# Kernel optimization log

Hardware: AMD Instinct MI355X
Metric: run time of the kernel (lower is better)

Reference implementation:

```python
import jax, jax.numpy as jnp
import numpy as np

N_IN = 100000   # active voxels at coarse level
N_OUT = 400000  # active voxels at fine level
K = 8           # 2x2x2 kernel offsets of the inverse conv
P = 100000      # rulebook pairs per kernel offset
C_IN, C_OUT, C_SKIP = 128, 64, 64
EPS = 1e-5


def setup_inputs() -> dict:
    key = jax.random.key(0)
    k1, k2, k3, k4, k5, k6 = jax.random.split(key, 6)
    x_feats = jax.random.normal(k1, (N_IN, C_IN), jnp.float32)
    skip_feats = jax.random.normal(k2, (N_OUT, C_SKIP), jnp.float32)
    W_deconv = jax.random.normal(k3, (K, C_IN, C_OUT), jnp.float32) * (1.0 / np.sqrt(C_IN * K))
    gamma = jnp.ones((C_OUT,), jnp.float32)
    beta = jnp.zeros((C_OUT,), jnp.float32)
    W_fuse = jax.random.normal(k4, (C_OUT + C_SKIP, C_OUT), jnp.float32) * (1.0 / np.sqrt(C_OUT + C_SKIP))
    in_idx = jax.random.randint(k5, (K, P), 0, N_IN, jnp.int32)
    out_idx = jax.random.randint(k6, (K, P), 0, N_OUT, jnp.int32)
    return {"x_feats": x_feats, "skip_feats": skip_feats, "W_deconv": W_deconv,
            "gamma": gamma, "beta": beta, "W_fuse": W_fuse,
            "in_idx": in_idx, "out_idx": out_idx}


def reference(x_feats, skip_feats, W_deconv, gamma, beta, W_fuse, in_idx, out_idx):
    # --- SparseInverseConv3d: gather-GEMM-scatter over the rulebook ---
    gathered = x_feats[in_idx]                                  # [K,P,C_IN]
    contrib = jnp.einsum('kpi,kio->kpo', gathered, W_deconv)    # [K,P,C_OUT]
    y = jnp.zeros((N_OUT, C_OUT), x_feats.dtype)
    y = y.at[out_idx.reshape(-1)].add(contrib.reshape(-1, C_OUT))
    # --- BatchNorm1d (batch stats, biased var) + ReLU on voxel features ---
    mean = jnp.mean(y, axis=0)
    var = jnp.mean((y - mean) ** 2, axis=0)
    y = (y - mean) * jax.lax.rsqrt(var + EPS) * gamma + beta
    y = jax.nn.relu(y)
    # --- channel concat with skip, then SubMConv3d(kernel=1) == linear ---
    z = jnp.concatenate([y, skip_feats], axis=1)                # [N_OUT, C_OUT+C_SKIP]
    return z @ W_fuse                                           # [N_OUT, C_OUT]
```

## Files before the change

kernel.cpp:

```cpp
#include <hip/hip_runtime.h>

#define N_IN   100000
#define N_OUT  400000
#define KK     8
#define PP     100000
#define C_IN   128
#define C_OUTC 64
#define C_SKIP 64
#define EPS_BN 1e-5f
#define SLOTS  16
#define GEMM_GRID 1024

typedef __attribute__((ext_vector_type(8))) short bf16x8;
typedef __attribute__((ext_vector_type(4))) float f32x4;

__device__ __forceinline__ unsigned short f2b(float f) {
    unsigned int u = __builtin_bit_cast(unsigned int, f);
    return (unsigned short)((u + 0x7FFFu + ((u >> 16) & 1u)) >> 16);
}
__device__ __forceinline__ float b2f(unsigned short v) {
    return __builtin_bit_cast(float, (unsigned)v << 16);
}

__global__ __launch_bounds__(256) void prep_all(
    const float* __restrict__ Wd, unsigned short* __restrict__ bfrag,
    int4* __restrict__ counts4, float4* __restrict__ mid4)
{
    const int t = blockIdx.x * 256 + threadIdx.x;
    if (t < N_OUT / 4)
        counts4[t] = (int4){0, 0, 0, 0};
    if (t < (32 * 128) / 4)
        mid4[t] = (float4){0.f, 0.f, 0.f, 0.f};
    if (t < KK * 4 * 4 * 64 * 8) {
        const int j  = t & 7;
        const int l  = (t >> 3) & 63;
        const int ct = (t >> 9) & 3;
        const int ks = (t >> 11) & 3;
        const int ko = t >> 13;
        const int i  = ks * 32 + (l >> 4) * 8 + j;
        const int c  = ct * 16 + (l & 15);
        bfrag[t] = f2b(Wd[((size_t)ko * C_IN + i) * C_OUTC + c]);
    }
}

__global__ __launch_bounds__(256) void fill_csr(
    const int* __restrict__ in_idx, const int* __restrict__ out_idx,
    int* __restrict__ counts, int* __restrict__ slots)
{
    const int q = blockIdx.x * 256 + threadIdx.x;
    if (q < KK * PP) {
        const int row = out_idx[q];
        const int pk  = in_idx[q] * KK + q / PP;
        const int idx = atomicAdd(&counts[row], 1);
        if (idx < SLOTS) slots[(size_t)row * SLOTS + idx] = pk;
    }
}

__global__ __launch_bounds__(256) void gemm_all(
    const float* __restrict__ x, const unsigned short* __restrict__ bfrag,
    unsigned short* __restrict__ z)
{
    __shared__ __align__(16) unsigned short lds[2][32 * 136];
    const int tid = threadIdx.x;
    const int wv  = tid >> 6;
    const int l   = tid & 63;
    const int r16 = l & 15, hi = l >> 4;
    const int ntiles = N_IN / 32;

    int t = blockIdx.x;
    float4 ld[4];
    {
        const float4* __restrict__ xt = (const float4*)(x + (size_t)t * 32 * C_IN);
        #pragma unroll
        for (int i = 0; i < 4; ++i) ld[i] = xt[i * 256 + tid];
    }
    #pragma unroll
    for (int i = 0; i < 4; ++i) {
        const int e = i * 256 + tid, row = e >> 5, q = e & 31;
        uint2 p;
        p.x = f2b(ld[i].x) | ((unsigned)f2b(ld[i].y) << 16);
        p.y = f2b(ld[i].z) | ((unsigned)f2b(ld[i].w) << 16);
        *(uint2*)(&lds[0][row * 136 + q * 4]) = p;
    }
    __syncthreads();
    int cur = 0;

    while (true) {
        const int tn = t + GEMM_GRID;
        const bool more = tn < ntiles;
        if (more) {
            const float4* __restrict__ xt = (const float4*)(x + (size_t)tn * 32 * C_IN);
            #pragma unroll
            for (int i = 0; i < 4; ++i) ld[i] = xt[i * 256 + tid];
        }

        const unsigned short* __restrict__ al = lds[cur];
        f32x4 acc[2][2][4];
        #pragma unroll
        for (int q = 0; q < 2; ++q)
            #pragma unroll
            for (int rt = 0; rt < 2; ++rt)
                #pragma unroll
                for (int ct = 0; ct < 4; ++ct)
                    acc[q][rt][ct] = (f32x4){0.f, 0.f, 0.f, 0.f};

        #pragma unroll
        for (int ks = 0; ks < 4; ++ks) {
            const bf16x8 a0 = *(const bf16x8*)(&al[r16 * 136 + ks * 32 + hi * 8]);
            const bf16x8 a1 = *(const bf16x8*)(&al[(16 + r16) * 136 + ks * 32 + hi * 8]);
            #pragma unroll
            for (int q = 0; q < 2; ++q) {
                const unsigned short* __restrict__ bk = bfrag + (size_t)(wv * 2 + q) * 8192;
                #pragma unroll
                for (int ct = 0; ct < 4; ++ct) {
                    const bf16x8 b = *(const bf16x8*)(bk + ((ks * 4 + ct) * 64 + l) * 8);
                    acc[q][0][ct] = __builtin_amdgcn_mfma_f32_16x16x32_bf16(a0, b, acc[q][0][ct], 0, 0, 0);
                    acc[q][1][ct] = __builtin_amdgcn_mfma_f32_16x16x32_bf16(a1, b, acc[q][1][ct], 0, 0, 0);
                }
            }
        }

        const int rb = t * 32;
        #pragma unroll
        for (int q = 0; q < 2; ++q) {
            const int k = wv * 2 + q;
            #pragma unroll
            for (int rt = 0; rt < 2; ++rt)
                #pragma unroll
                for (int ct = 0; ct < 4; ++ct)
                    #pragma unroll
                    for (int j = 0; j < 4; ++j)
                        z[((size_t)(rb + rt * 16 + hi * 4 + j) * KK + k) * 64 + ct * 16 + r16]
                            = f2b(acc[q][rt][ct][j]);
        }

        if (!more) break;

        #pragma unroll
        for (int i = 0; i < 4; ++i) {
            const int e = i * 256 + tid, row = e >> 5, q = e & 31;
            uint2 p;
            p.x = f2b(ld[i].x) | ((unsigned)f2b(ld[i].y) << 16);
            p.y = f2b(ld[i].z) | ((unsigned)f2b(ld[i].w) << 16);
            *(uint2*)(&lds[cur ^ 1][row * 136 + q * 4]) = p;
        }
        __syncthreads();
        cur ^= 1;
        t = tn;
    }
}

__global__ __launch_bounds__(512) void gather_yb(
    const unsigned short* __restrict__ z, const int* __restrict__ counts,
    const int* __restrict__ slots, unsigned short* __restrict__ yb,
    float* __restrict__ mid)
{
    const int tid = threadIdx.x, lane = tid & 63;
    const int gw  = (int)blockIdx.x * 8 + (tid >> 6);
    const int r0  = gw * 8;

    const int4 c0 = *(const int4*)(counts + r0);
    const int4 c1 = *(const int4*)(counts + r0 + 4);
    const int cnt[8] = {c0.x, c0.y, c0.z, c0.w, c1.x, c1.y, c1.z, c1.w};
    int4 s4[8];
    #pragma unroll
    for (int i = 0; i < 8; ++i)
        s4[i] = *(const int4*)(slots + (size_t)(r0 + i) * SLOTS);

    float ssum = 0.f, ssq = 0.f;
    float a[8];
    #pragma unroll
    for (int i = 0; i < 8; ++i) {
        const int c  = cnt[i] > SLOTS ? SLOTS : cnt[i];
        const int p0 = c > 0 ? s4[i].x : 0;
        const int p1 = c > 1 ? s4[i].y : 0;
        const int p2 = c > 2 ? s4[i].z : 0;
        const int p3 = c > 3 ? s4[i].w : 0;
        const float v0 = b2f(z[(size_t)p0 * 64 + lane]);
        const float v1 = b2f(z[(size_t)p1 * 64 + lane]);
        const float v2 = b2f(z[(size_t)p2 * 64 + lane]);
        const float v3 = b2f(z[(size_t)p3 * 64 + lane]);
        float s = (c > 0 ? v0 : 0.f) + (c > 1 ? v1 : 0.f);
        s += (c > 2 ? v2 : 0.f) + (c > 3 ? v3 : 0.f);
        if (c > 4) {
            for (int j = 4; j < c; ++j)
                s += b2f(z[(size_t)slots[(size_t)(r0 + i) * SLOTS + j] * 64 + lane]);
        }
        a[i] = s;
    }
    #pragma unroll
    for (int i = 0; i < 8; ++i) {
        yb[(size_t)(r0 + i) * C_OUTC + lane] = f2b(a[i]);
        ssum += a[i];
        ssq = fmaf(a[i], a[i], ssq);
    }

    __shared__ float rs[512], rq[512];
    rs[tid] = ssum; rq[tid] = ssq;
    __syncthreads();
    if (tid < 64) {
        float s = 0.f, q2 = 0.f;
        #pragma unroll
        for (int w = 0; w < 8; ++w) { s += rs[tid + w * 64]; q2 += rq[tid + w * 64]; }
        float* mrow = mid + (size_t)(blockIdx.x & 31) * 128;
        atomicAdd(&mrow[tid], s);
        atomicAdd(&mrow[64 + tid], q2);
    }
}

__global__ void finalize_p(const float* __restrict__ mid,
                           const float* __restrict__ gamma,
                           const float* __restrict__ beta,
                           const float* __restrict__ Wf,
                           float* __restrict__ sc,
                           unsigned short* __restrict__ wf_frag)
{
    __shared__ float acc2[128];
    __shared__ float bsh[C_OUTC];
    __shared__ float ssc[C_OUTC];
    const int t = threadIdx.x;
    float s = 0.f;
    #pragma unroll
    for (int b = 0; b < 32; ++b) s += mid[(size_t)b * 128 + t];
    acc2[t] = s;
    __syncthreads();
    if (t < 64) {
        const float inv_n = 1.0f / (float)N_OUT;
        const float mean  = acc2[t] * inv_n;
        const float var   = acc2[64 + t] * inv_n - mean * mean;
        const float sg    = gamma[t] * rsqrtf(var + EPS_BN);
        const float b     = beta[t] - mean * sg;
        sc[t]            = sg;
        sc[C_OUTC + t]   = -b / sg;
        ssc[t] = sg;
        bsh[t] = b;
    }
    __syncthreads();
    if (t < 64) {
        float acc = 0.f;
        for (int i = 0; i < C_OUTC; ++i)
            acc = fmaf(bsh[i], Wf[i * C_OUTC + t], acc);
        sc[2 * C_OUTC + t] = acc;
    }
    for (int e = t; e < 4 * 4 * 64 * 8; e += 128) {
        const int j  = e & 7;
        const int l  = (e >> 3) & 63;
        const int ct = (e >> 9) & 3;
        const int ks = e >> 11;
        const int i  = ks * 32 + (l >> 4) * 8 + j;
        const int c  = ct * 16 + (l & 15);
        float w = Wf[(size_t)i * C_OUTC + c];
        if (i < C_OUTC) w *= ssc[i];
        wf_frag[e] = f2b(w);
    }
}

__global__ __launch_bounds__(256) void fuse_mfma_b(
    const unsigned short* __restrict__ yb, const float* __restrict__ skip,
    const unsigned short* __restrict__ wf_frag, const float* __restrict__ sc,
    float* __restrict__ out)
{
    __shared__ __align__(16) unsigned short alds[128 * 136];
    __shared__ float nbsh[C_OUTC];
    const int rb = blockIdx.x * 128;
    if (threadIdx.x < C_OUTC) nbsh[threadIdx.x] = sc[C_OUTC + threadIdx.x];
    __syncthreads();

    const uint4* __restrict__ yb4 = (const uint4*)(yb + (size_t)rb * C_OUTC);
    for (int e = threadIdx.x; e < 128 * 8; e += 256) {
        const int row = e >> 3, q = e & 7;
        uint4 v = yb4[row * 8 + q];
        uint4 o;
        unsigned* vp = (unsigned*)&v;
        unsigned* op = (unsigned*)&o;
        #pragma unroll
        for (int h = 0; h < 4; ++h) {
            const float lo = fmaxf(b2f((unsigned short)(vp[h] & 0xFFFF)), nbsh[q * 8 + h * 2]);
            const float hf = fmaxf(b2f((unsigned short)(vp[h] >> 16)),    nbsh[q * 8 + h * 2 + 1]);
            op[h] = f2b(lo) | ((unsigned)f2b(hf) << 16);
        }
        *(uint4*)(&alds[row * 136 + q * 8]) = o;
    }
    const float4* __restrict__ s4 = (const float4*)(skip + (size_t)rb * C_SKIP);
    for (int e = threadIdx.x; e < 128 * 16; e += 256) {
        const int row = e >> 4, q = e & 15;
        const float4 v = s4[row * 16 + q];
        uint2 p;
        p.x = f2b(v.x) | ((unsigned)f2b(v.y) << 16);
        p.y = f2b(v.z) | ((unsigned)f2b(v.w) << 16);
        *(uint2*)(&alds[row * 136 + 64 + q * 4]) = p;
    }
    __syncthreads();

    const int w   = threadIdx.x >> 6;
    const int l   = threadIdx.x & 63;
    const int r16 = l & 15, hi = l >> 4;
    const int rw  = w * 32;

    f32x4 acc[2][4];
    #pragma unroll
    for (int ct = 0; ct < 4; ++ct) {
        const float b0 = sc[2 * C_OUTC + ct * 16 + r16];
        acc[0][ct] = (f32x4){b0, b0, b0, b0};
        acc[1][ct] = (f32x4){b0, b0, b0, b0};
    }

    #pragma unroll
    for (int ks = 0; ks < 4; ++ks) {
        const bf16x8 a0 = *(const bf16x8*)(&alds[(rw + r16) * 136 + ks * 32 + hi * 8]);
        const bf16x8 a1 = *(const bf16x8*)(&alds[(rw + 16 + r16) * 136 + ks * 32 + hi * 8]);
        #pragma unroll
        for (int ct = 0; ct < 4; ++ct) {
            const bf16x8 b = *(const bf16x8*)(wf_frag + ((ks * 4 + ct) * 64 + l) * 8);
            acc[0][ct] = __builtin_amdgcn_mfma_f32_16x16x32_bf16(a0, b, acc[0][ct], 0, 0, 0);
            acc[1][ct] = __builtin_amdgcn_mfma_f32_16x16x32_bf16(a1, b, acc[1][ct], 0, 0, 0);
        }
    }

    #pragma unroll
    for (int rt = 0; rt < 2; ++rt)
        #pragma unroll
        for (int ct = 0; ct < 4; ++ct)
            #pragma unroll
            for (int j = 0; j < 4; ++j)
                out[(size_t)(rb + rw + rt * 16 + hi * 4 + j) * C_OUTC + ct * 16 + r16]
                    = acc[rt][ct][j];
}

extern "C" void kernel_launch(void* const* d_in, const int* in_sizes, int n_in,
                              void* d_out, int out_size, void* d_ws, size_t ws_size,
                              hipStream_t stream)
{
    const float* x      = (const float*)d_in[0];
    const float* skip   = (const float*)d_in[1];
    const float* Wd     = (const float*)d_in[2];
    const float* gamma  = (const float*)d_in[3];
    const float* beta   = (const float*)d_in[4];
    const float* Wf     = (const float*)d_in[5];
    const int*   in_idx  = (const int*)d_in[6];
    const int*   out_idx = (const int*)d_in[7];

    float* y  = (float*)d_out;
    float* sc = (float*)d_ws + 128;

    char* p = (char*)d_ws + 4096;
    unsigned short* bfrag   = (unsigned short*)p;  p += (size_t)KK * 8192 * 2;
    unsigned short* wf_frag = (unsigned short*)p;  p += 8192 * 2;
    int*   counts   = (int*)p;                     p += (size_t)N_OUT * 4;
    int*   slots    = (int*)p;                     p += (size_t)N_OUT * SLOTS * 4;
    float* mid      = (float*)p;                   p += (size_t)32 * 128 * 4;
    unsigned short* z = (unsigned short*)p;        p += (size_t)N_IN * KK * C_OUTC * 2;
    unsigned short* yb = (unsigned short*)p;

    prep_all<<<(N_OUT / 4 + 255) / 256, 256, 0, stream>>>(
        Wd, bfrag, (int4*)counts, (float4*)mid);
    fill_csr<<<(KK * PP + 255) / 256, 256, 0, stream>>>(in_idx, out_idx, counts, slots);
    gemm_all<<<GEMM_GRID, 256, 0, stream>>>(x, bfrag, z);
    gather_yb<<<N_OUT / 64, 512, 0, stream>>>(z, counts, slots, yb, mid);
    finalize_p<<<1, 128, 0, stream>>>(mid, gamma, beta, Wf, sc, wf_frag);
    fuse_mfma_b<<<N_OUT / 128, 256, 0, stream>>>(yb, skip, wf_frag, sc, y);
}
```

Measured before the change: 244.8 us.

## Make fuse kernel persistent with double-buffered register prefetch; use 32-bit gather offsets

```diff
diff --git a/kernel.cpp b/kernel.cpp
--- a/kernel.cpp
+++ b/kernel.cpp
@@ -10,6 +10,7 @@
 #define EPS_BN 1e-5f
 #define SLOTS  16
 #define GEMM_GRID 1024
+#define FUSE_GRID 1024
 
 typedef __attribute__((ext_vector_type(8))) short bf16x8;
 typedef __attribute__((ext_vector_type(4))) float f32x4;
@@ -155,7 +156,8 @@
     const int* __restrict__ slots, unsigned short* __restrict__ yb,
     float* __restrict__ mid)
 {
-    const int tid = threadIdx.x, lane = tid & 63;
+    const int tid = threadIdx.x;
+    const unsigned lane = threadIdx.x & 63;
     const int gw  = (int)blockIdx.x * 8 + (tid >> 6);
     const int r0  = gw * 8;
 
@@ -172,25 +174,25 @@
     #pragma unroll
     for (int i = 0; i < 8; ++i) {
         const int c  = cnt[i] > SLOTS ? SLOTS : cnt[i];
-        const int p0 = c > 0 ? s4[i].x : 0;
-        const int p1 = c > 1 ? s4[i].y : 0;
-        const int p2 = c > 2 ? s4[i].z : 0;
-        const int p3 = c > 3 ? s4[i].w : 0;
-        const float v0 = b2f(z[(size_t)p0 * 64 + lane]);
-        const float v1 = b2f(z[(size_t)p1 * 64 + lane]);
-        const float v2 = b2f(z[(size_t)p2 * 64 + lane]);
-        const float v3 = b2f(z[(size_t)p3 * 64 + lane]);
+        const unsigned o0 = (unsigned)(c > 0 ? s4[i].x : 0) * 64u + lane;
+        const unsigned o1 = (unsigned)(c > 1 ? s4[i].y : 0) * 64u + lane;
+        const unsigned o2 = (unsigned)(c > 2 ? s4[i].z : 0) * 64u + lane;
+        const unsigned o3 = (unsigned)(c > 3 ? s4[i].w : 0) * 64u + lane;
+        const float v0 = b2f(z[o0]);
+        const float v1 = b2f(z[o1]);
+        const float v2 = b2f(z[o2]);
+        const float v3 = b2f(z[o3]);
         float s = (c > 0 ? v0 : 0.f) + (c > 1 ? v1 : 0.f);
         s += (c > 2 ? v2 : 0.f) + (c > 3 ? v3 : 0.f);
         if (c > 4) {
             for (int j = 4; j < c; ++j)
-                s += b2f(z[(size_t)slots[(size_t)(r0 + i) * SLOTS + j] * 64 + lane]);
+                s += b2f(z[(unsigned)slots[(size_t)(r0 + i) * SLOTS + j] * 64u + lane]);
         }
         a[i] = s;
     }
     #pragma unroll
     for (int i = 0; i < 8; ++i) {
-        yb[(size_t)(r0 + i) * C_OUTC + lane] = f2b(a[i]);
+        yb[(unsigned)(r0 + i) * 64u + lane] = f2b(a[i]);
         ssum += a[i];
         ssq = fmaf(a[i], a[i], ssq);
     }
@@ -260,17 +262,34 @@
     const unsigned short* __restrict__ wf_frag, const float* __restrict__ sc,
     float* __restrict__ out)
 {
-    __shared__ __align__(16) unsigned short alds[128 * 136];
+    __shared__ __align__(16) unsigned short alds[2][64 * 136];
     __shared__ float nbsh[C_OUTC];
-    const int rb = blockIdx.x * 128;
-    if (threadIdx.x < C_OUTC) nbsh[threadIdx.x] = sc[C_OUTC + threadIdx.x];
-    __syncthreads();
-
-    const uint4* __restrict__ yb4 = (const uint4*)(yb + (size_t)rb * C_OUTC);
-    for (int e = threadIdx.x; e < 128 * 8; e += 256) {
-        const int row = e >> 3, q = e & 7;
-        uint4 v = yb4[row * 8 + q];
-        uint4 o;
+    const int tid = threadIdx.x;
+    if (tid < C_OUTC) nbsh[tid] = sc[C_OUTC + tid];
+    __syncthreads();
+
+    const int ntiles = N_OUT / 64;
+    const int w   = tid >> 6;
+    const int l   = tid & 63;
+    const int r16 = l & 15, hi = l >> 4;
+    const int rw  = w * 16;
+
+    uint4  ly[2];
+    float4 lsk[4];
+    int t = blockIdx.x;
+
+    {
+        const uint4*  __restrict__ yt = (const uint4*)(yb + (size_t)t * 64 * C_OUTC);
+        const float4* __restrict__ st = (const float4*)(skip + (size_t)t * 64 * C_SKIP);
+        #pragma unroll
+        for (int i = 0; i < 2; ++i) ly[i] = yt[i * 256 + tid];
+        #pragma unroll
+        for (int i = 0; i < 4; ++i) lsk[i] = st[i * 256 + tid];
+    }
+    #pragma unroll
+    for (int i = 0; i < 2; ++i) {
+        const int e = i * 256 + tid, row = e >> 3, q = e & 7;
+        uint4 v = ly[i], o;
         unsigned* vp = (unsigned*)&v;
         unsigned* op = (unsigned*)&o;
         #pragma unroll
@@ -279,52 +298,86 @@
             const float hf = fmaxf(b2f((unsigned short)(vp[h] >> 16)),    nbsh[q * 8 + h * 2 + 1]);
             op[h] = f2b(lo) | ((unsigned)f2b(hf) << 16);
         }
-        *(uint4*)(&alds[row * 136 + q * 8]) = o;
-    }
-    const float4* __restrict__ s4 = (const float4*)(skip + (size_t)rb * C_SKIP);
-    for (int e = threadIdx.x; e < 128 * 16; e += 256) {
-        const int row = e >> 4, q = e & 15;
-        const float4 v = s4[row * 16 + q];
+        *(uint4*)(&alds[0][row * 136 + q * 8]) = o;
+    }
+    #pragma unroll
+    for (int i = 0; i < 4; ++i) {
+        const int e = i * 256 + tid, row = e >> 4, q = e & 15;
+        const float4 v = lsk[i];
         uint2 p;
         p.x = f2b(v.x) | ((unsigned)f2b(v.y) << 16);
         p.y = f2b(v.z) | ((unsigned)f2b(v.w) << 16);
-        *(uint2*)(&alds[row * 136 + 64 + q * 4]) = p;
-    }
-    __syncthreads();
-
-    const int w   = threadIdx.x >> 6;
-    const int l   = threadIdx.x & 63;
-    const int r16 = l & 15, hi = l >> 4;
-    const int rw  = w * 32;
-
-    f32x4 acc[2][4];
-    #pragma unroll
-    for (int ct = 0; ct < 4; ++ct) {
-        const float b0 = sc[2 * C_OUTC + ct * 16 + r16];
-        acc[0][ct] = (f32x4){b0, b0, b0, b0};
-        acc[1][ct] = (f32x4){b0, b0, b0, b0};
-    }
-
-    #pragma unroll
-    for (int ks = 0; ks < 4; ++ks) {
-        const bf16x8 a0 = *(const bf16x8*)(&alds[(rw + r16) * 136 + ks * 32 + hi * 8]);
-        const bf16x8 a1 = *(const bf16x8*)(&alds[(rw + 16 + r16) * 136 + ks * 32 + hi * 8]);
+        *(uint2*)(&alds[0][row * 136 + 64 + q * 4]) = p;
+    }
+    __syncthreads();
+    int cur = 0;
+
+    while (true) {
+        const int tn = t + FUSE_GRID;
+        const bool more = tn < ntiles;
+        if (more) {
+            const uint4*  __restrict__ yt = (const uint4*)(yb + (size_t)tn * 64 * C_OUTC);
+            const float4* __restrict__ st = (const float4*)(skip + (size_t)tn * 64 * C_SKIP);
+            #pragma unroll
+            for (int i = 0; i < 2; ++i) ly[i] = yt[i * 256 + tid];
+            #pragma unroll
+            for (int i = 0; i < 4; ++i) lsk[i] = st[i * 256 + tid];
+        }
+
+        const unsigned short* __restrict__ al = alds[cur];
+        f32x4 acc[4];
         #pragma unroll
         for (int ct = 0; ct < 4; ++ct) {
-            const bf16x8 b = *(const bf16x8*)(wf_frag + ((ks * 4 + ct) * 64 + l) * 8);
-            acc[0][ct] = __builtin_amdgcn_mfma_f32_16x16x32_bf16(a0, b, acc[0][ct], 0, 0, 0);
-            acc[1][ct] = __builtin_amdgcn_mfma_f32_16x16x32_bf16(a1, b, acc[1][ct], 0, 0, 0);
-        }
-    }
-
-    #pragma unroll
-    for (int rt = 0; rt < 2; ++rt)
+            const float b0 = sc[2 * C_OUTC + ct * 16 + r16];
+            acc[ct] = (f32x4){b0, b0, b0, b0};
+        }
+        #pragma unroll
+        for (int ks = 0; ks < 4; ++ks) {
+            const bf16x8 a0 = *(const bf16x8*)(&al[(rw + r16) * 136 + ks * 32 + hi * 8]);
+            #pragma unroll
+            for (int ct = 0; ct < 4; ++ct) {
+                const bf16x8 b = *(const bf16x8*)(wf_frag + ((ks * 4 + ct) * 64 + l) * 8);
+                acc[ct] = __builtin_amdgcn_mfma_f32_16x16x32_bf16(a0, b, acc[ct], 0, 0, 0);
+            }
+        }
+
+        const int rb = t * 64;
         #pragma unroll
         for (int ct = 0; ct < 4; ++ct)
             #pragma unroll
             for (int j = 0; j < 4; ++j)
-                out[(size_t)(rb + rw + rt * 16 + hi * 4 + j) * C_OUTC + ct * 16 + r16]
-                    = acc[rt][ct][j];
+                out[(size_t)(rb + rw + hi * 4 + j) * C_OUTC + ct * 16 + r16] = acc[ct][j];
+
+        if (!more) break;
+
+        unsigned short* __restrict__ dl = alds[cur ^ 1];
+        #pragma unroll
+        for (int i = 0; i < 2; ++i) {
+            const int e = i * 256 + tid, row = e >> 3, q = e & 7;
+            uint4 v = ly[i], o;
+            unsigned* vp = (unsigned*)&v;
+            unsigned* op = (unsigned*)&o;
+            #pragma unroll
+            for (int h = 0; h < 4; ++h) {
+                const float lo = fmaxf(b2f((unsigned short)(vp[h] & 0xFFFF)), nbsh[q * 8 + h * 2]);
+                const float hf = fmaxf(b2f((unsigned short)(vp[h] >> 16)),    nbsh[q * 8 + h * 2 + 1]);
+                op[h] = f2b(lo) | ((unsigned)f2b(hf) << 16);
+            }
+            *(uint4*)(&dl[row * 136 + q * 8]) = o;
+        }
+        #pragma unroll
+        for (int i = 0; i < 4; ++i) {
+            const int e = i * 256 + tid, row = e >> 4, q = e & 15;
+            const float4 v = lsk[i];
+            uint2 p;
+            p.x = f2b(v.x) | ((unsigned)f2b(v.y) << 16);
+            p.y = f2b(v.z) | ((unsigned)f2b(v.w) << 16);
+            *(uint2*)(&dl[row * 136 + 64 + q * 4]) = p;
+        }
+        __syncthreads();
+        cur ^= 1;
+        t = tn;
+    }
 }
 
 extern "C" void kernel_launch(void* const* d_in, const int* in_sizes, int n_in,
@@ -358,5 +411,5 @@
     gemm_all<<<GEMM_GRID, 256, 0, stream>>>(x, bfrag, z);
     gather_yb<<<N_OUT / 64, 512, 0, stream>>>(z, counts, slots, yb, mid);
     finalize_p<<<1, 128, 0, stream>>>(mid, gamma, beta, Wf, sc, wf_frag);
-    fuse_mfma_b<<<N_OUT / 128, 256, 0, stream>>>(yb, skip, wf_frag, sc, y);
-}
+    fuse_mfma_b<<<FUSE_GRID, 256, 0, stream>>>(yb, skip, wf_frag, sc, y);
+}
```

Result: faster. 222.9 us (-9.0%).
